# Kernel optimization log

Measured on AMD Instinct MI355X. Metric: run time of the kernel, lower is better.

## Reference

```python
import math
import jax, jax.numpy as jnp
import numpy as np

N, K, D = 500_000, 16, 8
TWO_PI = 2.0 * math.pi


def setup_inputs() -> dict:
    key = jax.random.key(0)
    k0, k1, k2, k3 = jax.random.split(key, 4)
    X = jax.random.normal(k0, (N, D), jnp.float32)
    mu = jax.random.normal(k1, (K, D), jnp.float32)
    L = jax.random.normal(k2, (K, D, D), jnp.float32) * 0.3
    # positive weights keep the (squared-weight) mixture pdf strictly positive
    weights = jax.random.uniform(k3, (K,), jnp.float32, 0.2, 1.0)
    return {"X": X, "mu": mu, "L": L, "weights": weights, "it": 0}


def reference(X, mu, L, weights, it):
    # Covariances via Cholesky composition: tril(L) @ tril(L)^T + I   [K,D,D]
    Lt = jnp.tril(L)
    sig = Lt @ jnp.swapaxes(Lt, -1, -2) + jnp.eye(D, dtype=X.dtype)
    prec = jnp.linalg.inv(sig)                     # sigma_k^{-1}      [K,D,D]

    # Pairwise squared params: P_ij = prec_i + prec_j, Sigma_ij = P_ij^{-1}
    P = prec[:, None] + prec[None, :]              # [K,K,D,D]
    Sig_pair = jnp.linalg.inv(P)                   # [K,K,D,D]
    rhs = jnp.einsum('kde,ke->kd', prec, mu)       # prec_k @ mu_k     [K,D]
    rp = rhs[:, None, :] + rhs[None, :, :]         # [K,K,D]
    mu_pair = jnp.einsum('ijde,ije->ijd', Sig_pair, rp)  # [K,K,D]

    # z_ij = 1/sqrt(det((2*pi)^D * Sigma_ij))  (faithful: scalar scales the matrix
    # before det, giving (2*pi)^(D*D) * det(Sigma))
    detS = jnp.linalg.det(Sig_pair)                # [K,K]
    z = 1.0 / jnp.sqrt((TWO_PI ** D) ** D * detS)  # [K,K]

    Pf = P.reshape(K * K, D * D)                   # [K^2, D^2]
    Xo = (X[:, :, None] * X[:, None, :]).reshape(-1, D * D)  # [N, D^2]
    xPx = Xo @ Pf.T                                # [N, K^2]
    b = jnp.einsum('ijde,ije->ijd', P, mu_pair).reshape(K * K, D)  # P mu  [K^2,D]
    xPmu = X @ b.T                                 # [N, K^2]
    muPmu = jnp.einsum('pd,pd->p', mu_pair.reshape(K * K, D), b)   # [K^2]
    quad = xPx - 2.0 * xPmu + muPmu[None, :]       # [N, K^2]

    wpair = (weights[:, None] * weights[None, :]).reshape(-1)      # [K^2]
    pdf = jnp.exp(-0.5 * quad) @ (z.reshape(-1) * wpair)           # [N]

    # Faithful quirk: original returns z * pdf where z is from the LAST (i,j)
    # pair, i.e. (K-1, K-1).
    z_last = z.reshape(-1)[-1]
    return jnp.log(z_last * pdf).mean()
```

## Files before the change

kernel.cpp:

```cpp
#include <hip/hip_runtime.h>
#include <math.h>


#define LOG2E_F 1.4426950408889634f
#define LN2_F   0.6931471805599453f
#define LN2PI_F 1.8378770664093453f

#define WS_COEF 0
#define WS_ES   768
#define WS_NSC  904
#define WS_K    960
#define WS_PART 1024

__device__ __forceinline__ float fexp2(float x) {
#if __has_builtin(__builtin_amdgcn_exp2f)
  return __builtin_amdgcn_exp2f(x);
#else
  return exp2f(x);
#endif
}
__device__ __forceinline__ float flog2(float x) {
#if __has_builtin(__builtin_amdgcn_logf)
  return __builtin_amdgcn_logf(x);
#else
  return log2f(x);
#endif
}

__device__ __forceinline__ void chol8(const float (*A)[8], float (*C)[8]) {
  #pragma unroll
  for (int d = 0; d < 8; ++d) {
    float s = A[d][d];
    #pragma unroll
    for (int m = 0; m < 8; ++m) if (m < d) s -= C[d][m] * C[d][m];
    float cd = sqrtf(s);
    C[d][d] = cd;
    float inv = 1.f / cd;
    #pragma unroll
    for (int e = 0; e < 8; ++e) if (e > d) {
      float t = A[e][d];
      #pragma unroll
      for (int m = 0; m < 8; ++m) if (m < d) t -= C[e][m] * C[d][m];
      C[e][d] = t * inv;
    }
  }
}

__global__ __launch_bounds__(256) void gm_setup(const float* __restrict__ mu,
                                                const float* __restrict__ L,
                                                const float* __restrict__ wts,
                                                float* __restrict__ ws) {
  __shared__ float sp[16][72];
  int tid = threadIdx.x;
  if (tid < 16) {
    int k = tid;
    float Lt[8][8];
    #pragma unroll
    for (int d = 0; d < 8; ++d)
      #pragma unroll
      for (int e = 0; e < 8; ++e)
        Lt[d][e] = (e <= d) ? L[k * 64 + d * 8 + e] : 0.f;
    float A[8][8];
    #pragma unroll
    for (int d = 0; d < 8; ++d)
      #pragma unroll
      for (int e = 0; e <= d; ++e) {
        float s = (d == e) ? 1.f : 0.f;
        #pragma unroll
        for (int m = 0; m < 8; ++m) s += Lt[d][m] * Lt[e][m];
        A[d][e] = s;
        A[e][d] = s;
      }
    float C[8][8];
    chol8(A, C);
    float Ci[8][8];
    #pragma unroll
    for (int d = 0; d < 8; ++d) Ci[d][d] = 1.f / C[d][d];
    #pragma unroll
    for (int e = 0; e < 8; ++e)
      #pragma unroll
      for (int d = 0; d < 8; ++d) if (d > e) {
        float s = 0.f;
        #pragma unroll
        for (int m = 0; m < 8; ++m) if (m >= e && m < d) s += C[d][m] * Ci[m][e];
        Ci[d][e] = -s * Ci[d][d];
      }
    #pragma unroll
    for (int a = 0; a < 8; ++a)
      #pragma unroll
      for (int b = 0; b < 8; ++b) {
        float s = 0.f;
        #pragma unroll
        for (int m = 0; m < 8; ++m) if (m >= a && m >= b) s += Ci[m][a] * Ci[m][b];
        sp[k][a * 8 + b] = s;
      }
    #pragma unroll
    for (int d = 0; d < 8; ++d) {
      float s = 0.f;
      #pragma unroll
      for (int e = 0; e < 8; ++e) s += sp[k][d * 8 + e] * mu[k * 8 + e];
      sp[k][64 + d] = s;
    }
  }
  __syncthreads();

  int p = tid;
  int i = p >> 4, j = p & 15;
  const float* pi = sp[i];
  const float* pj = sp[j];
  float P[8][8], rp[8];
  #pragma unroll
  for (int d = 0; d < 8; ++d) {
    #pragma unroll
    for (int e = 0; e < 8; ++e) P[d][e] = pi[d * 8 + e] + pj[d * 8 + e];
    rp[d] = pi[64 + d] + pj[64 + d];
  }
  float U[8][8];
  chol8(P, U);
  float logdet = 0.f;
  #pragma unroll
  for (int d = 0; d < 8; ++d) logdet += logf(U[d][d]);
  logdet *= 2.f;
  float zf[8];
  #pragma unroll
  for (int d = 0; d < 8; ++d) {
    float s = rp[d];
    #pragma unroll
    for (int m = 0; m < 8; ++m) if (m < d) s -= U[d][m] * zf[m];
    zf[d] = s / U[d][d];
  }
  float y[8];
  #pragma unroll
  for (int dd = 7; dd >= 0; --dd) {
    float s = zf[dd];
    #pragma unroll
    for (int m = 0; m < 8; ++m) if (m > dd) s -= U[m][dd] * y[m];
    y[dd] = s / U[dd][dd];
  }
  float muPmu = 0.f;
  #pragma unroll
  for (int d = 0; d < 8; ++d) muPmu += rp[d] * y[d];
  float c = -0.5f * muPmu + 0.5f * logdet - 32.f * LN2PI_F
          + logf(wts[i]) + logf(wts[j]) + 64.f * LN2_F;
  float Ev = expf(c);
  if (j <= i)
    ws[WS_ES + i * (i + 1) / 2 + j] = (i == j) ? Ev : 2.f * Ev;
  if (i == j) {
    float* c0 = ws + WS_COEF + i * 48;
    int q = 0;
    #pragma unroll
    for (int d = 0; d < 8; ++d) {
      c0[q++] = pi[64 + d] * LOG2E_F;
      #pragma unroll
      for (int e = d; e < 8; ++e) {
        float v = (d == e) ? -0.5f * pi[d * 8 + e] : -pi[d * 8 + e];
        c0[q++] = v * LOG2E_F;
      }
    }
    c0[44] = 0.f; c0[45] = 0.f; c0[46] = 0.f; c0[47] = 0.f;
  }
  if (p == 255) ws[WS_K] = 0.5f * logdet - 32.f * LN2PI_F - 64.f * LN2_F;
}

__global__ __launch_bounds__(256) void gm_main(const float* __restrict__ X,
                                               const float* __restrict__ cf,
                                               float* __restrict__ partials,
                                               int N) {
  __shared__ float sc[WS_NSC];
  for (int t = threadIdx.x; t < WS_NSC; t += 256) sc[t] = cf[t];

  const int gid = blockIdx.x * 256 + threadIdx.x;
  const bool act = gid < N;
  const int src = act ? gid : 0;
  const float4* Xv = reinterpret_cast<const float4*>(X) + (size_t)src * 2;
  float4 a = Xv[0], b = Xv[1];
  __syncthreads();
  float xs[8] = {a.x, a.y, a.z, a.w, b.x, b.y, b.z, b.w};

  float u[16];
  #pragma unroll
  for (int i = 0; i < 16; ++i) {
    const float* c = sc + i * 48;
    float g = 0.f;
    int q = 0;
    #pragma unroll
    for (int d = 0; d < 8; ++d) {
      float r = c[q++];
      #pragma unroll
      for (int e = d; e < 8; ++e) r = fmaf(c[q++], xs[e], r);
      g = fmaf(xs[d], r, g);
    }
    u[i] = fexp2(g);
  }

  float pdf = 0.f;
  #pragma unroll
  for (int i = 0; i < 16; ++i) {
    const float* e = sc + WS_ES + (i * (i + 1)) / 2;
    float s0 = 0.f, s1 = 0.f;
    #pragma unroll
    for (int j = 0; j + 1 <= i; j += 2) {
      s0 = fmaf(e[j + 0], u[j + 0], s0);
      s1 = fmaf(e[j + 1], u[j + 1], s1);
    }
    if (!(i & 1)) s0 = fmaf(e[i], u[i], s0);
    pdf = fmaf(u[i], s0 + s1, pdf);
  }
  float lsum = act ? flog2(pdf) : 0.f;

  #pragma unroll
  for (int off = 32; off > 0; off >>= 1) lsum += __shfl_down(lsum, off, 64);
  __shared__ float wsum[4];
  int lane = threadIdx.x & 63, wid = threadIdx.x >> 6;
  if (lane == 0) wsum[wid] = lsum;
  __syncthreads();
  if (threadIdx.x == 0)
    partials[blockIdx.x] = (wsum[0] + wsum[1]) + (wsum[2] + wsum[3]);
}

__global__ __launch_bounds__(256) void gm_final(const float* __restrict__ ws,
                                                float* __restrict__ out,
                                                int nb, float invN) {
  const float* partials = ws + WS_PART;
  float s = 0.f;
  for (int t = threadIdx.x; t < nb; t += 256) s += partials[t];
  #pragma unroll
  for (int off = 32; off > 0; off >>= 1) s += __shfl_down(s, off, 64);
  __shared__ float wsum[4];
  int lane = threadIdx.x & 63, wid = threadIdx.x >> 6;
  if (lane == 0) wsum[wid] = s;
  __syncthreads();
  if (threadIdx.x == 0) {
    float tot = (wsum[0] + wsum[1]) + (wsum[2] + wsum[3]);
    out[0] = tot * LN2_F * invN + ws[WS_K];
  }
}

extern "C" void kernel_launch(void* const* d_in, const int* in_sizes, int n_in,
                              void* d_out, int out_size, void* d_ws, size_t ws_size,
                              hipStream_t stream) {
  const float* X = (const float*)d_in[0];
  const float* mu = (const float*)d_in[1];
  const float* L = (const float*)d_in[2];
  const float* wts = (const float*)d_in[3];
  float* ws = (float*)d_ws;
  float* out = (float*)d_out;
  int N = in_sizes[0] / 8;
  int nb = (N + 255) / 256;
  gm_setup<<<1, 256, 0, stream>>>(mu, L, wts, ws);
  gm_main<<<nb, 256, 0, stream>>>(X, ws, ws + WS_PART, N);
  gm_final<<<1, 256, 0, stream>>>(ws, out, nb, 1.0f / (float)N);
}
```

Measured before the change: 29.46 us.

## Process two points per thread with packed float2 FMAs and vectorized LDS coefficient loads

Each thread now handles two samples, packing their coordinates into float2 vectors so the quadratic-form and mixture-sum FMAs can map to packed FP32 instructions. Coefficients are loaded from LDS as float4, and the triangular pair-weight table is padded to 4-aligned rows (zero-filled in setup) so it can also be read as float4. The grid is halved. This trades extra register pressure and some wasted zero-multiplies in the padded rows for fewer LDS loads, fewer instructions per sample, and fewer blocks.

```diff
diff --git a/kernel.cpp b/kernel.cpp
--- a/kernel.cpp
+++ b/kernel.cpp
@@ -8,9 +8,12 @@
 
 #define WS_COEF 0
 #define WS_ES   768
-#define WS_NSC  904
-#define WS_K    960
-#define WS_PART 1024
+#define WS_K    1024
+#define WS_PART 1088
+
+typedef float f2 __attribute__((ext_vector_type(2)));
+
+__device__ const int EOFF_D[16] = {0,4,8,12,16,24,32,40,48,60,72,84,96,112,128,144};
 
 __device__ __forceinline__ float fexp2(float x) {
 #if __has_builtin(__builtin_amdgcn_exp2f)
@@ -26,6 +29,9 @@
   return log2f(x);
 #endif
 }
+__device__ __forceinline__ f2 vfma(float c, f2 x, f2 a) {
+  return __builtin_elementwise_fma((f2){c, c}, x, a);
+}
 
 __device__ __forceinline__ void chol8(const float (*A)[8], float (*C)[8]) {
   #pragma unroll
@@ -52,6 +58,7 @@
                                                 float* __restrict__ ws) {
   __shared__ float sp[16][72];
   int tid = threadIdx.x;
+  ws[768 + tid] = 0.f;
   if (tid < 16) {
     int k = tid;
     float Lt[8][8];
@@ -144,7 +151,7 @@
           + logf(wts[i]) + logf(wts[j]) + 64.f * LN2_F;
   float Ev = expf(c);
   if (j <= i)
-    ws[WS_ES + i * (i + 1) / 2 + j] = (i == j) ? Ev : 2.f * Ev;
+    ws[WS_ES + EOFF_D[i] + j] = (i == j) ? Ev : 2.f * Ev;
   if (i == j) {
     float* c0 = ws + WS_COEF + i * 48;
     int q = 0;
@@ -166,47 +173,91 @@
                                                const float* __restrict__ cf,
                                                float* __restrict__ partials,
                                                int N) {
-  __shared__ float sc[WS_NSC];
-  for (int t = threadIdx.x; t < WS_NSC; t += 256) sc[t] = cf[t];
-
-  const int gid = blockIdx.x * 256 + threadIdx.x;
-  const bool act = gid < N;
-  const int src = act ? gid : 0;
-  const float4* Xv = reinterpret_cast<const float4*>(X) + (size_t)src * 2;
-  float4 a = Xv[0], b = Xv[1];
+  __shared__ float sc[1024];
+  {
+    const float4* cf4 = reinterpret_cast<const float4*>(cf);
+    reinterpret_cast<float4*>(sc)[threadIdx.x] = cf4[threadIdx.x];
+  }
+
+  const int t = threadIdx.x;
+  const int g0i = blockIdx.x * 512 + t;
+  const int g1i = g0i + 256;
+  const bool act0 = g0i < N, act1 = g1i < N;
+  const float4* Xv0 = reinterpret_cast<const float4*>(X) + (size_t)(act0 ? g0i : 0) * 2;
+  const float4* Xv1 = reinterpret_cast<const float4*>(X) + (size_t)(act1 ? g1i : 0) * 2;
+  float4 a0 = Xv0[0], b0 = Xv0[1];
+  float4 a1 = Xv1[0], b1 = Xv1[1];
   __syncthreads();
-  float xs[8] = {a.x, a.y, a.z, a.w, b.x, b.y, b.z, b.w};
-
-  float u[16];
+
+  f2 xs[8];
+  xs[0] = (f2){a0.x, a1.x}; xs[1] = (f2){a0.y, a1.y};
+  xs[2] = (f2){a0.z, a1.z}; xs[3] = (f2){a0.w, a1.w};
+  xs[4] = (f2){b0.x, b1.x}; xs[5] = (f2){b0.y, b1.y};
+  xs[6] = (f2){b0.z, b1.z}; xs[7] = (f2){b0.w, b1.w};
+
+  constexpr int D_OF[44] = {0,0,0,0,0,0,0,0,0,
+                            1,1,1,1,1,1,1,1,
+                            2,2,2,2,2,2,2,
+                            3,3,3,3,3,3,
+                            4,4,4,4,4,
+                            5,5,5,5,
+                            6,6,6,
+                            7,7};
+  constexpr int E_OF[44] = {-1,0,1,2,3,4,5,6,7,
+                            -1,1,2,3,4,5,6,7,
+                            -1,2,3,4,5,6,7,
+                            -1,3,4,5,6,7,
+                            -1,4,5,6,7,
+                            -1,5,6,7,
+                            -1,6,7,
+                            -1,7};
+
+  f2 u[16];
   #pragma unroll
   for (int i = 0; i < 16; ++i) {
-    const float* c = sc + i * 48;
-    float g = 0.f;
-    int q = 0;
-    #pragma unroll
-    for (int d = 0; d < 8; ++d) {
-      float r = c[q++];
-      #pragma unroll
-      for (int e = d; e < 8; ++e) r = fmaf(c[q++], xs[e], r);
-      g = fmaf(xs[d], r, g);
-    }
-    u[i] = fexp2(g);
-  }
-
-  float pdf = 0.f;
+    const float4* c4 = reinterpret_cast<const float4*>(sc + i * 48);
+    f2 g = (f2){0.f, 0.f};
+    f2 r = (f2){0.f, 0.f};
+    #pragma unroll
+    for (int v = 0; v < 11; ++v) {
+      float4 w = c4[v];
+      #pragma unroll
+      for (int k2 = 0; k2 < 4; ++k2) {
+        const int q = 4 * v + k2;
+        const float cc = (k2 == 0) ? w.x : (k2 == 1) ? w.y : (k2 == 2) ? w.z : w.w;
+        if (E_OF[q] < 0) {
+          if (q > 0) g = __builtin_elementwise_fma(xs[D_OF[q - 1]], r, g);
+          r = (f2){cc, cc};
+        } else {
+          r = vfma(cc, xs[E_OF[q]], r);
+        }
+      }
+    }
+    g = __builtin_elementwise_fma(xs[7], r, g);
+    u[i] = (f2){fexp2(g.x), fexp2(g.y)};
+  }
+
+  constexpr int EOFF[16]  = {0,4,8,12,16,24,32,40,48,60,72,84,96,112,128,144};
+  constexpr int ELEN4[16] = {1,1,1,1,2,2,2,2,3,3,3,3,4,4,4,4};
+  const float4* es4 = reinterpret_cast<const float4*>(sc + 768);
+  f2 pdf = (f2){0.f, 0.f};
   #pragma unroll
   for (int i = 0; i < 16; ++i) {
-    const float* e = sc + WS_ES + (i * (i + 1)) / 2;
-    float s0 = 0.f, s1 = 0.f;
-    #pragma unroll
-    for (int j = 0; j + 1 <= i; j += 2) {
-      s0 = fmaf(e[j + 0], u[j + 0], s0);
-      s1 = fmaf(e[j + 1], u[j + 1], s1);
-    }
-    if (!(i & 1)) s0 = fmaf(e[i], u[i], s0);
-    pdf = fmaf(u[i], s0 + s1, pdf);
-  }
-  float lsum = act ? flog2(pdf) : 0.f;
+    f2 s = (f2){0.f, 0.f};
+    #pragma unroll
+    for (int q4 = 0; q4 < ELEN4[i]; ++q4) {
+      float4 ev = es4[EOFF[i] / 4 + q4];
+      const int j = q4 * 4;
+      s = vfma(ev.x, u[j + 0], s);
+      s = vfma(ev.y, u[j + 1], s);
+      s = vfma(ev.z, u[j + 2], s);
+      s = vfma(ev.w, u[j + 3], s);
+    }
+    pdf = __builtin_elementwise_fma(u[i], s, pdf);
+  }
+  float lsum = 0.f;
+  if (act0) lsum += flog2(pdf.x);
+  if (act1) lsum += flog2(pdf.y);
 
   #pragma unroll
   for (int off = 32; off > 0; off >>= 1) lsum += __shfl_down(lsum, off, 64);
@@ -246,7 +297,7 @@
   float* ws = (float*)d_ws;
   float* out = (float*)d_out;
   int N = in_sizes[0] / 8;
-  int nb = (N + 255) / 256;
+  int nb = (N + 511) / 512;
   gm_setup<<<1, 256, 0, stream>>>(mu, L, wts, ws);
   gm_main<<<nb, 256, 0, stream>>>(X, ws, ws + WS_PART, N);
   gm_final<<<1, 256, 0, stream>>>(ws, out, nb, 1.0f / (float)N);
```

Result: faster. 26.04 us (-11.6%).
